# Optimization experiments

Measured on AMD Instinct MI355X. Metric: run time of the kernel, lower is better.

Reference implementation:

```python
import jax, jax.numpy as jnp
import numpy as np

TAU = 0.2
ALPHA = 0.8
LAM_POS = 1.5  # extrapolation lambda (hard positives)
EPS = 1e-8


def _cosine_sim(e):
    # torch F.cosine_similarity with eps=1e-8 norm clamping
    n = jnp.maximum(jnp.linalg.norm(e, axis=1), EPS)
    return (e @ e.T) / (n[:, None] * n[None, :])


def setup_inputs() -> dict:
    key = jax.random.key(0)
    N, D = 4096, 128
    emb = jax.random.normal(key, (N, D), dtype=jnp.float32)
    k = jnp.arange(N // 2, dtype=jnp.int32)
    i, j = 2 * k, 2 * k + 1
    # disjoint positive pairs, both orientations (matches symmetric set semantics)
    pp = jnp.concatenate([jnp.stack([i, j], 1), jnp.stack([j, i], 1)], 0)
    return {"embeddings": emb, "positive_pairs": pp, "stage_train": 1}


def reference(embeddings, positive_pairs, stage_train):
    N = embeddings.shape[0]
    pi, pj = positive_pairs[:, 0], positive_pairs[:, 1]
    Mp = jnp.zeros((N, N), dtype=bool).at[pi, pj].set(True)  # symmetric (both dirs in pairs)
    eye = jnp.eye(N, dtype=bool)
    Mn = (~eye) & (~Mp)  # negative pair mask

    # hard positive extrapolation: 1.5*e_i - 0.5*e_j (pairs disjoint -> order-free)
    hard_pos = jnp.zeros_like(embeddings).at[pi].set(
        LAM_POS * embeddings[pi] + (1.0 - LAM_POS) * embeddings[pj])

    # hard negative interpolation: loop over negatives in row-major order, last write
    idx = jnp.arange(N, dtype=jnp.int32)
    posmat = idx[:, None] * N + idx[None, :]          # enumeration position of pair (i,j)
    A = jnp.where(Mn, posmat, -1)
    col_max, col_arg = A.max(axis=0), A.argmax(axis=0)  # m as second element of (i,m)
    row_max, row_arg = A.max(axis=1), A.argmax(axis=1)  # m as first element of (m,j)
    partner = jnp.where(col_max > row_max, col_arg, row_arg)
    hard_neg = 0.5 * (embeddings + embeddings[partner])

    sim = _cosine_sim(embeddings)
    sim = jnp.where(Mp, _cosine_sim(hard_pos), jnp.where(Mn, _cosine_sim(hard_neg), sim))

    # contrastive loss with quantile hard mining
    mask = eye | Mp
    exp_sim = jnp.exp(sim / TAU)
    exp_masked = jnp.where(mask, 0.0, exp_sim)
    pos_ij = exp_sim[pi, pj]
    pos_ji = exp_sim[pj, pi]
    ei = exp_masked[pi]  # [2P, N]
    ej = exp_masked[pj]
    if stage_train:
        ti = jnp.quantile(ei, ALPHA, axis=1, keepdims=True)
        tj = jnp.quantile(ej, ALPHA, axis=1, keepdims=True)
        si = jnp.where(ei >= ti, ei, 0.0).sum(axis=1)
        sj = jnp.where(ej >= tj, ej, 0.0).sum(axis=1)
    else:
        si = ei.sum(axis=1)
        sj = ej.sum(axis=1)
    loss_ij = -jnp.log(pos_ij / (pos_ij + si))
    loss_ji = -jnp.log(pos_ji / (pos_ji + sj))
    num_pairs = positive_pairs.shape[0]
    return (loss_ij + loss_ji).sum() / (2 * num_pairs)
```

## Files before the change

kernel.cpp:

```cpp
#include <hip/hip_runtime.h>
#include <hip/hip_bf16.h>
#include <math.h>

#define D 128
#define INV_TAU 5.0f

typedef short bf16x8 __attribute__((ext_vector_type(8)));
typedef unsigned short u16x8 __attribute__((ext_vector_type(8)));
typedef float f32x4 __attribute__((ext_vector_type(4)));

__global__ void scatter_pos(const int* __restrict__ pp, int* __restrict__ pos,
                            float* __restrict__ out, int K) {
    int k = blockIdx.x * blockDim.x + threadIdx.x;
    if (k == 0) *out = 0.0f;
    if (k < K) pos[pp[2 * k]] = pp[2 * k + 1];
}

__global__ void prep_kernel(const float* __restrict__ emb, const int* __restrict__ pos,
                            const int* __restrict__ pp, unsigned short* __restrict__ hnn,
                            float* __restrict__ hpn, int N) {
    int b = blockIdx.x, d = threadIdx.x;
    __shared__ int sP;
    __shared__ float tmp[2];
    bool isHn = (b < N);
    if (isHn && d == 0) {
        int r = b, posr = pos[r];
        int jmax = -1;
        for (int j = N - 1; j >= 0; --j) {
            if (j != r && j != posr) { jmax = j; break; }
        }
        int imax = -1;
        for (int i = N - 1; i >= 0; --i) {
            if (i != r && pos[i] != r) { imax = i; break; }
        }
        long long rowm = (jmax >= 0) ? (long long)r * N + jmax : -1;
        long long colm = (imax >= 0) ? (long long)imax * N + r : -1;
        sP = (colm > rowm) ? (imax < 0 ? 0 : imax) : (jmax < 0 ? 0 : jmax);
    }
    __syncthreads();
    float h;
    int outrow;
    if (isHn) {
        int p = sP;
        h = 0.5f * (emb[b * D + d] + emb[p * D + d]);
        outrow = b;
    } else {
        int k = b - N;
        int a = pp[2 * k], bb = pp[2 * k + 1];
        h = 1.5f * emb[a * D + d] - 0.5f * emb[bb * D + d];
        outrow = a;
    }
    float ss = h * h;
#pragma unroll
    for (int off = 32; off > 0; off >>= 1) ss += __shfl_down(ss, off);
    if ((d & 63) == 0) tmp[d >> 6] = ss;
    __syncthreads();
    float inv = 1.0f / fmaxf(sqrtf(tmp[0] + tmp[1]), 1e-8f);
    if (isHn) {
        __hip_bfloat16 hb = __float2bfloat16(h * inv);
        hnn[outrow * D + d] = *(unsigned short*)&hb;
    } else {
        hpn[outrow * D + d] = h * inv;
    }
}

__global__ __launch_bounds__(256) void gemm_sim(const unsigned short* __restrict__ hnn,
                                                const int* __restrict__ pos,
                                                unsigned short* __restrict__ sims, int N) {
    __shared__ unsigned short As[128 * 136];
    __shared__ unsigned short Bs[128 * 136];
    __shared__ int pos_s[128];
    int tid = threadIdx.x;
    int rowBase = blockIdx.y * 128, colBase = blockIdx.x * 128;
    if (tid < 128) pos_s[tid] = pos[rowBase + tid];

    u16x8 ra[8], rb[8];
#pragma unroll
    for (int i = 0; i < 8; ++i) {
        int idx = i * 256 + tid;
        int row = idx >> 4, seg = idx & 15;
        ra[i] = *(const u16x8*)&hnn[(size_t)(rowBase + row) * D + seg * 8];
        rb[i] = *(const u16x8*)&hnn[(size_t)(colBase + row) * D + seg * 8];
    }
#pragma unroll
    for (int i = 0; i < 8; ++i) {
        int idx = i * 256 + tid;
        int row = idx >> 4, seg = idx & 15;
        *(u16x8*)&As[row * 136 + seg * 8] = ra[i];
        *(u16x8*)&Bs[row * 136 + seg * 8] = rb[i];
    }
    __syncthreads();

    int wave = tid >> 6, lane = tid & 63;
    int quad = lane >> 4, l15 = lane & 15;
    int rowhalf = wave >> 1, colhalf = wave & 1;

    f32x4 acc[4][4] = {};
#pragma unroll
    for (int kk = 0; kk < 4; ++kk) {
        bf16x8 af[4], bf[4];
#pragma unroll
        for (int rt = 0; rt < 4; ++rt)
            af[rt] = *(const bf16x8*)&As[(rowhalf * 64 + rt * 16 + l15) * 136 + kk * 32 + quad * 8];
#pragma unroll
        for (int ct = 0; ct < 4; ++ct)
            bf[ct] = *(const bf16x8*)&Bs[(colhalf * 64 + ct * 16 + l15) * 136 + kk * 32 + quad * 8];
#pragma unroll
        for (int rt = 0; rt < 4; ++rt)
#pragma unroll
            for (int ct = 0; ct < 4; ++ct)
                acc[rt][ct] = __builtin_amdgcn_mfma_f32_16x16x32_bf16(af[rt], bf[ct],
                                                                     acc[rt][ct], 0, 0, 0);
    }

#pragma unroll
    for (int rt = 0; rt < 4; ++rt) {
#pragma unroll
        for (int rg = 0; rg < 4; ++rg) {
            int rloc = rowhalf * 64 + rt * 16 + quad * 4 + rg;
            int r = rowBase + rloc;
            int pr = pos_s[rloc];
#pragma unroll
            for (int ct = 0; ct < 4; ++ct) {
                int c = colBase + colhalf * 64 + ct * 16 + l15;
                float v = acc[rt][ct][rg];
                __hip_bfloat16 hb = __float2bfloat16(v);
                unsigned short u = *(unsigned short*)&hb;
                if (c == r || c == pr) u = 0xFF7F;
                sims[(size_t)r * N + c] = u;
            }
        }
    }
}

__global__ __launch_bounds__(512) void select_kernel(const unsigned short* __restrict__ sims,
                                                     const int* __restrict__ stage,
                                                     float* __restrict__ s_out, int N, int q) {
    int wave = threadIdx.x >> 6, lane = threadIdx.x & 63;
    int row = blockIdx.x * 8 + wave;
    const unsigned short* rp = sims + (size_t)row * N;

    unsigned s[64];
#pragma unroll
    for (int j = 0; j < 8; ++j) {
        u16x8 t = *(const u16x8*)&rp[j * 512 + lane * 8];
#pragma unroll
        for (int e = 0; e < 8; ++e) {
            unsigned u = (unsigned)(unsigned short)t[e];
            s[j * 8 + e] = (u & 0x8000u) ? (~u & 0xFFFFu) : (u | 0x8000u);
        }
    }

    unsigned T = 0;
    if (stage[0]) {
#pragma unroll
        for (int b = 15; b >= 0; --b) {
            unsigned cand = T | (1u << b);
            int cnt = 0;
#pragma unroll
            for (int i = 0; i < 64; ++i) cnt += (s[i] < cand);
#pragma unroll
            for (int off = 1; off < 64; off <<= 1) cnt += __shfl_xor(cnt, off);
            if (cnt <= q) T = cand;
        }
    }

    float sum = 0.0f;
#pragma unroll
    for (int i = 0; i < 64; ++i) {
        if (s[i] >= T) {
            unsigned u = (s[i] & 0x8000u) ? (s[i] ^ 0x8000u) : (~s[i] & 0xFFFFu);
            float f = __uint_as_float(u << 16);
            sum += __expf(f * INV_TAU);
        }
    }
#pragma unroll
    for (int off = 1; off < 64; off <<= 1) sum += __shfl_xor(sum, off);
    if (lane == 0) s_out[row] = sum;
}

__global__ __launch_bounds__(1024) void loss_kernel(const float* __restrict__ hpn,
                                                    const float* __restrict__ s,
                                                    const int* __restrict__ pp,
                                                    float* __restrict__ out, int K,
                                                    float scale) {
    int wave = threadIdx.x >> 6, lane = threadIdx.x & 63;
    int k = blockIdx.x * 16 + wave;
    float part = 0.0f;
    if (k < K) {
        int a = pp[2 * k], b = pp[2 * k + 1];
        float dsum = hpn[a * D + lane] * hpn[b * D + lane] +
                     hpn[a * D + lane + 64] * hpn[b * D + lane + 64];
#pragma unroll
        for (int off = 32; off > 0; off >>= 1) dsum += __shfl_down(dsum, off);
        if (lane == 0) {
            float p = __expf(dsum * INV_TAU);
            part = log1pf(s[a] / p) + log1pf(s[b] / p);
        }
    }
    __shared__ float red[16];
    if (lane == 0) red[wave] = part;
    __syncthreads();
    if (threadIdx.x == 0) {
        float tot = 0.0f;
#pragma unroll
        for (int w = 0; w < 16; ++w) tot += red[w];
        atomicAdd(out, tot * scale);
    }
}

extern "C" void kernel_launch(void* const* d_in, const int* in_sizes, int n_in,
                              void* d_out, int out_size, void* d_ws, size_t ws_size,
                              hipStream_t stream) {
    const float* emb = (const float*)d_in[0];
    const int* pp = (const int*)d_in[1];
    const int* stage = (const int*)d_in[2];
    int N = in_sizes[0] / D;
    int K = in_sizes[1] / 2;

    char* ws = (char*)d_ws;
    size_t offPos = 0;
    size_t offHnn = offPos + (size_t)N * 4;
    size_t offHpn = offHnn + (size_t)N * D * 2;
    size_t offS = offHpn + (size_t)N * D * 4;
    size_t offSims = offS + (size_t)N * 4;
    int* pos = (int*)(ws + offPos);
    unsigned short* hnn = (unsigned short*)(ws + offHnn);
    float* hpn = (float*)(ws + offHpn);
    float* s = (float*)(ws + offS);
    unsigned short* sims = (unsigned short*)(ws + offSims);

    scatter_pos<<<(K + 255) / 256, 256, 0, stream>>>(pp, pos, (float*)d_out, K);
    prep_kernel<<<N + K, D, 0, stream>>>(emb, pos, pp, hnn, hpn, N);
    dim3 g(N / 128, N / 128);
    gemm_sim<<<g, 256, 0, stream>>>(hnn, pos, sims, N);
    int q = (int)(0.8 * (double)(N - 1));
    select_kernel<<<N / 8, 512, 0, stream>>>(sims, stage, s, N, q);
    loss_kernel<<<(K + 15) / 16, 1024, 0, stream>>>(hpn, s, pp, (float*)d_out, K,
                                                    1.0f / (2.0f * K));
}
```

Before: 122.7 us.

## Fuse all stages into one cooperative persistent kernel with grid syncs

Replaces the five kernel launches with a single cooperative kernel of 512 blocks that runs scatter, prep, the GEMM, selection and the loss as phases separated by grid.sync. The GEMM is re-tiled to persistent 64x128 tiles. The sign-flip key transform for the radix select now happens in the GEMM epilogue instead of the select phase. The goal is to remove launch gaps and inter-kernel overhead, at the cost of grid-wide barriers, fewer parallel blocks per phase and smaller GEMM tiles; the old launches are kept as a fallback if the cooperative launch fails.

```diff
diff --git a/kernel.cpp b/kernel.cpp
--- a/kernel.cpp
+++ b/kernel.cpp
@@ -1,6 +1,9 @@
 #include <hip/hip_runtime.h>
 #include <hip/hip_bf16.h>
+#include <hip/hip_cooperative_groups.h>
 #include <math.h>
+
+namespace cg = cooperative_groups;
 
 #define D 128
 #define INV_TAU 5.0f
@@ -9,16 +12,225 @@
 typedef unsigned short u16x8 __attribute__((ext_vector_type(8)));
 typedef float f32x4 __attribute__((ext_vector_type(4)));
 
-__global__ void scatter_pos(const int* __restrict__ pp, int* __restrict__ pos,
-                            float* __restrict__ out, int K) {
+__device__ __forceinline__ unsigned short bf16_bits(float v) {
+    __hip_bfloat16 hb = __float2bfloat16(v);
+    return *(unsigned short*)&hb;
+}
+
+__global__ __launch_bounds__(512, 4) void mega_kernel(
+    const float* __restrict__ emb, const int* __restrict__ pp,
+    const int* __restrict__ stage, int* __restrict__ pos,
+    unsigned short* __restrict__ hnn, float* __restrict__ hpn,
+    float* __restrict__ s_out, unsigned short* __restrict__ sims,
+    float* __restrict__ out, int N, int K, int q) {
+    __shared__ unsigned short As[64 * 136];
+    __shared__ unsigned short Bs[128 * 136];
+    __shared__ int pos_s[64];
+    __shared__ float redf[16];
+
+    cg::grid_group grid = cg::this_grid();
+    int tid = threadIdx.x;
+    int wv = tid >> 6, lane = tid & 63;
+    int quad = lane >> 4, l15 = lane & 15;
+
+    for (int k = blockIdx.x * 512 + tid; k < K; k += gridDim.x * 512)
+        pos[pp[2 * k]] = pp[2 * k + 1];
+    if (blockIdx.x == 0 && tid == 0) *out = 0.0f;
+    grid.sync();
+
+    {
+        int g = tid >> 7, dd = tid & 127;
+        int rowsPer = gridDim.x * 4;
+        int total = N + K;
+        int iters = (total + rowsPer - 1) / rowsPer;
+        for (int it = 0; it < iters; ++it) {
+            int r = it * rowsPer + blockIdx.x * 4 + g;
+            bool act = r < total;
+            bool isHn = act && (r < N);
+            if (isHn && dd == 0) {
+                int rr = r, posr = pos[rr];
+                int jmax = -1;
+                for (int j = N - 1; j >= 0; --j)
+                    if (j != rr && j != posr) { jmax = j; break; }
+                int imax = -1;
+                for (int i = N - 1; i >= 0; --i)
+                    if (i != rr && pos[i] != rr) { imax = i; break; }
+                long long rowm = (jmax >= 0) ? (long long)rr * N + jmax : -1;
+                long long colm = (imax >= 0) ? (long long)imax * N + rr : -1;
+                pos_s[g] = (colm > rowm) ? (imax < 0 ? 0 : imax) : (jmax < 0 ? 0 : jmax);
+            }
+            __syncthreads();
+            float h = 0.0f;
+            int outrow = 0;
+            if (act) {
+                if (isHn) {
+                    int p = pos_s[g];
+                    h = 0.5f * (emb[r * D + dd] + emb[p * D + dd]);
+                    outrow = r;
+                } else {
+                    int kk2 = r - N;
+                    int a = pp[2 * kk2], bb = pp[2 * kk2 + 1];
+                    h = 1.5f * emb[a * D + dd] - 0.5f * emb[bb * D + dd];
+                    outrow = a;
+                }
+            }
+            float ss = h * h;
+#pragma unroll
+            for (int off = 32; off > 0; off >>= 1) ss += __shfl_down(ss, off);
+            if (lane == 0) redf[wv] = ss;
+            __syncthreads();
+            if (act) {
+                float inv = 1.0f / fmaxf(sqrtf(redf[g * 2] + redf[g * 2 + 1]), 1e-8f);
+                if (isHn)
+                    hnn[(size_t)outrow * D + dd] = bf16_bits(h * inv);
+                else
+                    hpn[(size_t)outrow * D + dd] = h * inv;
+            }
+            __syncthreads();
+        }
+    }
+    grid.sync();
+
+    {
+        int nTilesCol = N >> 7;
+        int totalTiles = (N >> 6) * nTilesCol;
+        int rowg = wv >> 2, colg = wv & 3;
+        for (int t = blockIdx.x; t < totalTiles; t += gridDim.x) {
+            int trow = t / nTilesCol, tcol = t - trow * nTilesCol;
+            int rowBase = trow * 64, colBase = tcol * 128;
+            __syncthreads();
+            if (tid < 64) pos_s[tid] = pos[rowBase + tid];
+#pragma unroll
+            for (int i = 0; i < 2; ++i) {
+                int idx = i * 512 + tid;
+                int row = idx >> 4, seg = idx & 15;
+                *(u16x8*)&As[row * 136 + seg * 8] =
+                    *(const u16x8*)&hnn[(size_t)(rowBase + row) * D + seg * 8];
+            }
+#pragma unroll
+            for (int i = 0; i < 4; ++i) {
+                int idx = i * 512 + tid;
+                int row = idx >> 4, seg = idx & 15;
+                *(u16x8*)&Bs[row * 136 + seg * 8] =
+                    *(const u16x8*)&hnn[(size_t)(colBase + row) * D + seg * 8];
+            }
+            __syncthreads();
+            f32x4 acc[2][2] = {};
+#pragma unroll
+            for (int kk = 0; kk < 4; ++kk) {
+                bf16x8 af[2], bf[2];
+#pragma unroll
+                for (int rt = 0; rt < 2; ++rt)
+                    af[rt] = *(const bf16x8*)&As[(rowg * 32 + rt * 16 + l15) * 136 + kk * 32 + quad * 8];
+#pragma unroll
+                for (int ct = 0; ct < 2; ++ct)
+                    bf[ct] = *(const bf16x8*)&Bs[(colg * 32 + ct * 16 + l15) * 136 + kk * 32 + quad * 8];
+#pragma unroll
+                for (int rt = 0; rt < 2; ++rt)
+#pragma unroll
+                    for (int ct = 0; ct < 2; ++ct)
+                        acc[rt][ct] = __builtin_amdgcn_mfma_f32_16x16x32_bf16(
+                            af[rt], bf[ct], acc[rt][ct], 0, 0, 0);
+            }
+#pragma unroll
+            for (int rt = 0; rt < 2; ++rt) {
+#pragma unroll
+                for (int rg = 0; rg < 4; ++rg) {
+                    int rloc = rowg * 32 + rt * 16 + quad * 4 + rg;
+                    int r = rowBase + rloc;
+                    int pr = pos_s[rloc];
+#pragma unroll
+                    for (int ct = 0; ct < 2; ++ct) {
+                        int c = colBase + colg * 32 + ct * 16 + l15;
+                        unsigned short u = bf16_bits(acc[rt][ct][rg]);
+                        unsigned short sv = (u & 0x8000u) ? (unsigned short)~u
+                                                          : (unsigned short)(u | 0x8000u);
+                        if (c == r || c == pr) sv = 0x0080;
+                        sims[(size_t)r * N + c] = sv;
+                    }
+                }
+            }
+        }
+    }
+    grid.sync();
+
+    {
+        int st = stage[0];
+        int row = blockIdx.x * 8 + wv;
+        if (row < N) {
+            const unsigned short* rp = sims + (size_t)row * N;
+            unsigned sarr[64];
+#pragma unroll
+            for (int j = 0; j < 8; ++j) {
+                u16x8 tv = *(const u16x8*)&rp[j * 512 + lane * 8];
+#pragma unroll
+                for (int e = 0; e < 8; ++e) sarr[j * 8 + e] = (unsigned)(unsigned short)tv[e];
+            }
+            unsigned T = 0;
+            if (st) {
+#pragma unroll
+                for (int b = 15; b >= 0; --b) {
+                    unsigned cand = T | (1u << b);
+                    int cnt = 0;
+#pragma unroll
+                    for (int i = 0; i < 64; ++i) cnt += (sarr[i] < cand);
+#pragma unroll
+                    for (int off = 1; off < 64; off <<= 1) cnt += __shfl_xor(cnt, off);
+                    if (cnt <= q) T = cand;
+                }
+            }
+            float sum = 0.0f;
+#pragma unroll
+            for (int i = 0; i < 64; ++i) {
+                if (sarr[i] >= T) {
+                    unsigned raw = (sarr[i] & 0x8000u) ? (sarr[i] ^ 0x8000u)
+                                                       : (~sarr[i] & 0xFFFFu);
+                    float f = __uint_as_float(raw << 16);
+                    sum += __expf(f * INV_TAU);
+                }
+            }
+#pragma unroll
+            for (int off = 1; off < 64; off <<= 1) sum += __shfl_xor(sum, off);
+            if (lane == 0) s_out[row] = sum;
+        }
+    }
+    grid.sync();
+
+    {
+        float part = 0.0f;
+        int k = blockIdx.x * 8 + wv;
+        if (k < K) {
+            int a = pp[2 * k], b = pp[2 * k + 1];
+            float dsum = hpn[a * D + lane] * hpn[b * D + lane] +
+                         hpn[a * D + lane + 64] * hpn[b * D + lane + 64];
+#pragma unroll
+            for (int off = 32; off > 0; off >>= 1) dsum += __shfl_down(dsum, off);
+            if (lane == 0) {
+                float p = __expf(dsum * INV_TAU);
+                part = log1pf(s_out[a] / p) + log1pf(s_out[b] / p);
+            }
+        }
+        if (lane == 0) redf[wv] = part;
+        __syncthreads();
+        if (tid == 0) {
+            float tot = 0.0f;
+#pragma unroll
+            for (int w = 0; w < 8; ++w) tot += redf[w];
+            atomicAdd(out, tot / (2.0f * (float)K));
+        }
+    }
+}
+
+__global__ void scatter_pos_f(const int* __restrict__ pp, int* __restrict__ pos,
+                              float* __restrict__ out, int K) {
     int k = blockIdx.x * blockDim.x + threadIdx.x;
     if (k == 0) *out = 0.0f;
     if (k < K) pos[pp[2 * k]] = pp[2 * k + 1];
 }
 
-__global__ void prep_kernel(const float* __restrict__ emb, const int* __restrict__ pos,
-                            const int* __restrict__ pp, unsigned short* __restrict__ hnn,
-                            float* __restrict__ hpn, int N) {
+__global__ void prep_kernel_f(const float* __restrict__ emb, const int* __restrict__ pos,
+                              const int* __restrict__ pp, unsigned short* __restrict__ hnn,
+                              float* __restrict__ hpn, int N) {
     int b = blockIdx.x, d = threadIdx.x;
     __shared__ int sP;
     __shared__ float tmp[2];
@@ -26,13 +238,11 @@
     if (isHn && d == 0) {
         int r = b, posr = pos[r];
         int jmax = -1;
-        for (int j = N - 1; j >= 0; --j) {
+        for (int j = N - 1; j >= 0; --j)
             if (j != r && j != posr) { jmax = j; break; }
-        }
         int imax = -1;
-        for (int i = N - 1; i >= 0; --i) {
+        for (int i = N - 1; i >= 0; --i)
             if (i != r && pos[i] != r) { imax = i; break; }
-        }
         long long rowm = (jmax >= 0) ? (long long)r * N + jmax : -1;
         long long colm = (imax >= 0) ? (long long)imax * N + r : -1;
         sP = (colm > rowm) ? (imax < 0 ? 0 : imax) : (jmax < 0 ? 0 : jmax);
@@ -56,24 +266,21 @@
     if ((d & 63) == 0) tmp[d >> 6] = ss;
     __syncthreads();
     float inv = 1.0f / fmaxf(sqrtf(tmp[0] + tmp[1]), 1e-8f);
-    if (isHn) {
-        __hip_bfloat16 hb = __float2bfloat16(h * inv);
-        hnn[outrow * D + d] = *(unsigned short*)&hb;
-    } else {
+    if (isHn)
+        hnn[outrow * D + d] = bf16_bits(h * inv);
+    else
         hpn[outrow * D + d] = h * inv;
-    }
-}
-
-__global__ __launch_bounds__(256) void gemm_sim(const unsigned short* __restrict__ hnn,
-                                                const int* __restrict__ pos,
-                                                unsigned short* __restrict__ sims, int N) {
+}
+
+__global__ __launch_bounds__(256) void gemm_sim_f(const unsigned short* __restrict__ hnn,
+                                                  const int* __restrict__ pos,
+                                                  unsigned short* __restrict__ sims, int N) {
     __shared__ unsigned short As[128 * 136];
     __shared__ unsigned short Bs[128 * 136];
     __shared__ int pos_s[128];
     int tid = threadIdx.x;
     int rowBase = blockIdx.y * 128, colBase = blockIdx.x * 128;
     if (tid < 128) pos_s[tid] = pos[rowBase + tid];
-
     u16x8 ra[8], rb[8];
 #pragma unroll
     for (int i = 0; i < 8; ++i) {
@@ -90,11 +297,9 @@
         *(u16x8*)&Bs[row * 136 + seg * 8] = rb[i];
     }
     __syncthreads();
-
     int wave = tid >> 6, lane = tid & 63;
     int quad = lane >> 4, l15 = lane & 15;
     int rowhalf = wave >> 1, colhalf = wave & 1;
-
     f32x4 acc[4][4] = {};
 #pragma unroll
     for (int kk = 0; kk < 4; ++kk) {
@@ -112,7 +317,6 @@
                 acc[rt][ct] = __builtin_amdgcn_mfma_f32_16x16x32_bf16(af[rt], bf[ct],
                                                                      acc[rt][ct], 0, 0, 0);
     }
-
 #pragma unroll
     for (int rt = 0; rt < 4; ++rt) {
 #pragma unroll
@@ -123,9 +327,7 @@
 #pragma unroll
             for (int ct = 0; ct < 4; ++ct) {
                 int c = colBase + colhalf * 64 + ct * 16 + l15;
-                float v = acc[rt][ct][rg];
-                __hip_bfloat16 hb = __float2bfloat16(v);
-                unsigned short u = *(unsigned short*)&hb;
+                unsigned short u = bf16_bits(acc[rt][ct][rg]);
                 if (c == r || c == pr) u = 0xFF7F;
                 sims[(size_t)r * N + c] = u;
             }
@@ -133,13 +335,12 @@
     }
 }
 
-__global__ __launch_bounds__(512) void select_kernel(const unsigned short* __restrict__ sims,
-                                                     const int* __restrict__ stage,
-                                                     float* __restrict__ s_out, int N, int q) {
+__global__ __launch_bounds__(512) void select_kernel_f(const unsigned short* __restrict__ sims,
+                                                       const int* __restrict__ stage,
+                                                       float* __restrict__ s_out, int N, int q) {
     int wave = threadIdx.x >> 6, lane = threadIdx.x & 63;
     int row = blockIdx.x * 8 + wave;
     const unsigned short* rp = sims + (size_t)row * N;
-
     unsigned s[64];
 #pragma unroll
     for (int j = 0; j < 8; ++j) {
@@ -150,7 +351,6 @@
             s[j * 8 + e] = (u & 0x8000u) ? (~u & 0xFFFFu) : (u | 0x8000u);
         }
     }
-
     unsigned T = 0;
     if (stage[0]) {
 #pragma unroll
@@ -164,14 +364,12 @@
             if (cnt <= q) T = cand;
         }
     }
-
     float sum = 0.0f;
 #pragma unroll
     for (int i = 0; i < 64; ++i) {
         if (s[i] >= T) {
             unsigned u = (s[i] & 0x8000u) ? (s[i] ^ 0x8000u) : (~s[i] & 0xFFFFu);
-            float f = __uint_as_float(u << 16);
-            sum += __expf(f * INV_TAU);
+            sum += __expf(__uint_as_float(u << 16) * INV_TAU);
         }
     }
 #pragma unroll
@@ -179,11 +377,11 @@
     if (lane == 0) s_out[row] = sum;
 }
 
-__global__ __launch_bounds__(1024) void loss_kernel(const float* __restrict__ hpn,
-                                                    const float* __restrict__ s,
-                                                    const int* __restrict__ pp,
-                                                    float* __restrict__ out, int K,
-                                                    float scale) {
+__global__ __launch_bounds__(1024) void loss_kernel_f(const float* __restrict__ hpn,
+                                                      const float* __restrict__ s,
+                                                      const int* __restrict__ pp,
+                                                      float* __restrict__ out, int K,
+                                                      float scale) {
     int wave = threadIdx.x >> 6, lane = threadIdx.x & 63;
     int k = blockIdx.x * 16 + wave;
     float part = 0.0f;
@@ -229,13 +427,19 @@
     float* hpn = (float*)(ws + offHpn);
     float* s = (float*)(ws + offS);
     unsigned short* sims = (unsigned short*)(ws + offSims);
-
-    scatter_pos<<<(K + 255) / 256, 256, 0, stream>>>(pp, pos, (float*)d_out, K);
-    prep_kernel<<<N + K, D, 0, stream>>>(emb, pos, pp, hnn, hpn, N);
-    dim3 g(N / 128, N / 128);
-    gemm_sim<<<g, 256, 0, stream>>>(hnn, pos, sims, N);
+    float* out = (float*)d_out;
     int q = (int)(0.8 * (double)(N - 1));
-    select_kernel<<<N / 8, 512, 0, stream>>>(sims, stage, s, N, q);
-    loss_kernel<<<(K + 15) / 16, 1024, 0, stream>>>(hpn, s, pp, (float*)d_out, K,
-                                                    1.0f / (2.0f * K));
-}
+
+    void* args[] = {&emb, &pp, &stage, &pos, &hnn, &hpn, &s, &sims, &out, &N, &K, &q};
+    hipError_t err = hipLaunchCooperativeKernel((const void*)mega_kernel, dim3(512),
+                                                dim3(512), args, 0, stream);
+    if (err != hipSuccess) {
+        scatter_pos_f<<<(K + 255) / 256, 256, 0, stream>>>(pp, pos, out, K);
+        prep_kernel_f<<<N + K, D, 0, stream>>>(emb, pos, pp, hnn, hpn, N);
+        dim3 g(N / 128, N / 128);
+        gemm_sim_f<<<g, 256, 0, stream>>>(hnn, pos, sims, N);
+        select_kernel_f<<<N / 8, 512, 0, stream>>>(sims, stage, s, N, q);
+        loss_kernel_f<<<(K + 15) / 16, 1024, 0, stream>>>(hpn, s, pp, out, K,
+                                                          1.0f / (2.0f * K));
+    }
+}
```

Result: slower. 320.7 us (+161.4%).
